# Optimization experiments

Measured on AMD Instinct MI355X. Metric: run time of the kernel, lower is better.

The kernel has to match this reference:

```python
import jax, jax.numpy as jnp
import numpy as np

S = 100  # spatial_encoding_size

def setup_inputs() -> dict:
    key = jax.random.key(0)
    k1, k2 = jax.random.split(key)
    N, C, B = 1000000, 64, 32
    agent_encodings = jax.random.normal(k1, (N, C), dtype=jnp.float32)
    encode_coordinates = jax.random.randint(k2, (N,), 0, B * S * S, dtype=jnp.int64)
    return {"batch_size": B, "agent_encodings": agent_encodings, "encode_coordinates": encode_coordinates}

def reference(batch_size, agent_encodings, encode_coordinates):
    N, C = agent_encodings.shape
    num_seg = batch_size * S * S
    # max over all agents mapped to each flat grid cell (-inf for empty cells)
    seg_max = jax.ops.segment_max(agent_encodings, encode_coordinates, num_segments=num_seg)
    counts = jax.ops.segment_sum(jnp.ones((N,), dtype=agent_encodings.dtype), encode_coordinates, num_segments=num_seg)
    occupied = counts > 0
    grid = jnp.where(occupied[:, None], seg_max, jnp.zeros((), dtype=agent_encodings.dtype))
    grid = grid.reshape(batch_size, S, S, C)
    return jnp.transpose(grid, (0, 3, 1, 2))  # [B, C, S, S]
```

## Files before the change

### kernel.cpp

```cpp
#include <hip/hip_runtime.h>
#include <math.h>


#define S_DIM 100
#define CELLS_PER_B (S_DIM * S_DIM)
#define C_DIM 64

__global__ void build_lists(const int* __restrict__ coords,
                            int* __restrict__ head, int* __restrict__ next,
                            int n) {
    const int stride = gridDim.x * blockDim.x;
    for (int i = blockIdx.x * blockDim.x + threadIdx.x; i < n; i += stride) {
        const int c = coords[i];
        next[i] = atomicExch(&head[c], i);
    }
}

__global__ void gather_max(const float* __restrict__ enc,
                           const int* __restrict__ head,
                           const int* __restrict__ next,
                           float* __restrict__ out, int ncells) {
    __shared__ float tile[16][C_DIM + 1];
    const int tid = threadIdx.x;
    const int cl = tid >> 4;
    const int c4 = (tid & 15) << 2;
    const int cell = blockIdx.x * 16 + cl;

    float4 m = make_float4(-INFINITY, -INFINITY, -INFINITY, -INFINITY);
    int agent = (cell < ncells) ? head[cell] : -1;
    const bool occupied = (agent >= 0);
    while (agent >= 0) {
        const float4 v =
            *reinterpret_cast<const float4*>(enc + (size_t)agent * C_DIM + c4);
        m.x = fmaxf(m.x, v.x);
        m.y = fmaxf(m.y, v.y);
        m.z = fmaxf(m.z, v.z);
        m.w = fmaxf(m.w, v.w);
        agent = next[agent];
    }
    if (!occupied) m = make_float4(0.f, 0.f, 0.f, 0.f);
    tile[cl][c4 + 0] = m.x;
    tile[cl][c4 + 1] = m.y;
    tile[cl][c4 + 2] = m.z;
    tile[cl][c4 + 3] = m.w;
    __syncthreads();

    const int cell0 = blockIdx.x * 16;
    const int b = cell0 / CELLS_PER_B;
    const int rem0 = cell0 - b * CELLS_PER_B;
    float* base = out + ((size_t)b * C_DIM) * CELLS_PER_B + rem0;
    for (int i = tid; i < 16 * C_DIM; i += 256) {
        const int c = i >> 4;
        const int j = i & 15;
        if (cell0 + j < ncells)
            base[(size_t)c * CELLS_PER_B + j] = tile[j][c];
    }
}

__device__ __forceinline__ unsigned encode_f32(float f) {
    unsigned u = __float_as_uint(f);
    return (u & 0x80000000u) ? ~u : (u | 0x80000000u);
}
__device__ __forceinline__ float decode_key(unsigned k) {
    if (k == 0u) return 0.0f;
    return (k & 0x80000000u) ? __uint_as_float(k & 0x7FFFFFFFu)
                             : __uint_as_float(~k);
}
__global__ void spatial_scatter_max(const float* __restrict__ enc,
                                    const int* __restrict__ coords,
                                    unsigned* __restrict__ grid,
                                    int n_agents, int C) {
    const long long total = (long long)n_agents * 16;
    const long long stride = (long long)gridDim.x * blockDim.x;
    for (long long i = (long long)blockIdx.x * blockDim.x + threadIdx.x;
         i < total; i += stride) {
        const int agent = (int)(i >> 4);
        const int c4 = ((int)i & 15) << 2;
        const int coord = coords[agent];
        const int b = coord / CELLS_PER_B;
        const int rem = coord - b * CELLS_PER_B;
        const float4 v =
            *reinterpret_cast<const float4*>(enc + (size_t)agent * C + c4);
        unsigned* p = grid + ((size_t)b * C + c4) * CELLS_PER_B + rem;
        atomicMax(p, encode_f32(v.x));
        atomicMax(p + 1 * CELLS_PER_B, encode_f32(v.y));
        atomicMax(p + 2 * CELLS_PER_B, encode_f32(v.z));
        atomicMax(p + 3 * CELLS_PER_B, encode_f32(v.w));
    }
}
__global__ void spatial_decode(unsigned* __restrict__ grid, int n4) {
    const int stride = gridDim.x * blockDim.x;
    uint4* g4 = reinterpret_cast<uint4*>(grid);
    for (int i = blockIdx.x * blockDim.x + threadIdx.x; i < n4; i += stride) {
        uint4 k = g4[i];
        float4 f;
        f.x = decode_key(k.x);
        f.y = decode_key(k.y);
        f.z = decode_key(k.z);
        f.w = decode_key(k.w);
        reinterpret_cast<float4*>(g4)[i] = f;
    }
}

extern "C" void kernel_launch(void* const* d_in, const int* in_sizes, int n_in,
                              void* d_out, int out_size, void* d_ws, size_t ws_size,
                              hipStream_t stream) {
    const float* enc = (const float*)d_in[1];
    const int* coords = (const int*)d_in[2];
    const int n = in_sizes[2];
    const int ncells = out_size / C_DIM;

    const size_t need = (size_t)ncells * 4 + (size_t)n * 4;
    if (ws_size >= need) {
        int* head = (int*)d_ws;
        int* next = head + ncells;
        hipMemsetAsync(head, 0xFF, (size_t)ncells * 4, stream);
        build_lists<<<2048, 256, 0, stream>>>(coords, head, next, n);
        gather_max<<<(ncells + 15) / 16, 256, 0, stream>>>(
            enc, head, next, (float*)d_out, ncells);
    } else {
        unsigned* out = (unsigned*)d_out;
        hipMemsetAsync(d_out, 0, (size_t)out_size * sizeof(float), stream);
        spatial_scatter_max<<<2048, 256, 0, stream>>>(enc, coords, out, n,
                                                      C_DIM);
        spatial_decode<<<2048, 256, 0, stream>>>(out, out_size / 4);
    }
}
```

Measured before the change: 131.5 us.

## Widen gather tiles to 32 cells, use 2D grid, prefetch next pointer

The gather kernel now handles 32 cells per 512-thread block on a 2D grid indexed by batch and cell chunk, so each channel row is written in 32-float contiguous runs and no integer division is needed. It also loads the next-pointer before the encoding row, so walking the linked list overlaps with the feature load. The memset is replaced by a small init kernel and the atomic-scatter fallback is removed, which assumes the workspace is always large enough. Tiles that span the boundary between batches are now clipped correctly.

After: 132.5 us. About the same (+0.7%).

```diff
diff --git a/kernel.cpp b/kernel.cpp
--- a/kernel.cpp
+++ b/kernel.cpp
@@ -5,6 +5,13 @@
 #define S_DIM 100
 #define CELLS_PER_B (S_DIM * S_DIM)
 #define C_DIM 64
+#define CPB 32
+
+__global__ void init_head(int* __restrict__ head, int n) {
+    const int stride = gridDim.x * blockDim.x;
+    for (int i = blockIdx.x * blockDim.x + threadIdx.x; i < n; i += stride)
+        head[i] = -1;
+}
 
 __global__ void build_lists(const int* __restrict__ coords,
                             int* __restrict__ head, int* __restrict__ next,
@@ -16,27 +23,29 @@
     }
 }
 
-__global__ void gather_max(const float* __restrict__ enc,
-                           const int* __restrict__ head,
-                           const int* __restrict__ next,
-                           float* __restrict__ out, int ncells) {
-    __shared__ float tile[16][C_DIM + 1];
+__global__ __launch_bounds__(512) void gather_max(
+    const float* __restrict__ enc, const int* __restrict__ head,
+    const int* __restrict__ next, float* __restrict__ out) {
+    __shared__ float tile[CPB][C_DIM + 1];
     const int tid = threadIdx.x;
     const int cl = tid >> 4;
     const int c4 = (tid & 15) << 2;
-    const int cell = blockIdx.x * 16 + cl;
+    const int b = blockIdx.y;
+    const int rem0 = blockIdx.x * CPB;
+    const int rem = rem0 + cl;
 
     float4 m = make_float4(-INFINITY, -INFINITY, -INFINITY, -INFINITY);
-    int agent = (cell < ncells) ? head[cell] : -1;
+    int agent = (rem < CELLS_PER_B) ? head[b * CELLS_PER_B + rem] : -1;
     const bool occupied = (agent >= 0);
     while (agent >= 0) {
+        const int nxt = next[agent];
         const float4 v =
             *reinterpret_cast<const float4*>(enc + (size_t)agent * C_DIM + c4);
         m.x = fmaxf(m.x, v.x);
         m.y = fmaxf(m.y, v.y);
         m.z = fmaxf(m.z, v.z);
         m.w = fmaxf(m.w, v.w);
-        agent = next[agent];
+        agent = nxt;
     }
     if (!occupied) m = make_float4(0.f, 0.f, 0.f, 0.f);
     tile[cl][c4 + 0] = m.x;
@@ -45,60 +54,12 @@
     tile[cl][c4 + 3] = m.w;
     __syncthreads();
 
-    const int cell0 = blockIdx.x * 16;
-    const int b = cell0 / CELLS_PER_B;
-    const int rem0 = cell0 - b * CELLS_PER_B;
     float* base = out + ((size_t)b * C_DIM) * CELLS_PER_B + rem0;
-    for (int i = tid; i < 16 * C_DIM; i += 256) {
-        const int c = i >> 4;
-        const int j = i & 15;
-        if (cell0 + j < ncells)
-            base[(size_t)c * CELLS_PER_B + j] = tile[j][c];
-    }
-}
-
-__device__ __forceinline__ unsigned encode_f32(float f) {
-    unsigned u = __float_as_uint(f);
-    return (u & 0x80000000u) ? ~u : (u | 0x80000000u);
-}
-__device__ __forceinline__ float decode_key(unsigned k) {
-    if (k == 0u) return 0.0f;
-    return (k & 0x80000000u) ? __uint_as_float(k & 0x7FFFFFFFu)
-                             : __uint_as_float(~k);
-}
-__global__ void spatial_scatter_max(const float* __restrict__ enc,
-                                    const int* __restrict__ coords,
-                                    unsigned* __restrict__ grid,
-                                    int n_agents, int C) {
-    const long long total = (long long)n_agents * 16;
-    const long long stride = (long long)gridDim.x * blockDim.x;
-    for (long long i = (long long)blockIdx.x * blockDim.x + threadIdx.x;
-         i < total; i += stride) {
-        const int agent = (int)(i >> 4);
-        const int c4 = ((int)i & 15) << 2;
-        const int coord = coords[agent];
-        const int b = coord / CELLS_PER_B;
-        const int rem = coord - b * CELLS_PER_B;
-        const float4 v =
-            *reinterpret_cast<const float4*>(enc + (size_t)agent * C + c4);
-        unsigned* p = grid + ((size_t)b * C + c4) * CELLS_PER_B + rem;
-        atomicMax(p, encode_f32(v.x));
-        atomicMax(p + 1 * CELLS_PER_B, encode_f32(v.y));
-        atomicMax(p + 2 * CELLS_PER_B, encode_f32(v.z));
-        atomicMax(p + 3 * CELLS_PER_B, encode_f32(v.w));
-    }
-}
-__global__ void spatial_decode(unsigned* __restrict__ grid, int n4) {
-    const int stride = gridDim.x * blockDim.x;
-    uint4* g4 = reinterpret_cast<uint4*>(grid);
-    for (int i = blockIdx.x * blockDim.x + threadIdx.x; i < n4; i += stride) {
-        uint4 k = g4[i];
-        float4 f;
-        f.x = decode_key(k.x);
-        f.y = decode_key(k.y);
-        f.z = decode_key(k.z);
-        f.w = decode_key(k.w);
-        reinterpret_cast<float4*>(g4)[i] = f;
+    const int limit = min(CPB, CELLS_PER_B - rem0);
+    for (int i = tid; i < CPB * C_DIM; i += 512) {
+        const int c = i >> 5;
+        const int j = i & 31;
+        if (j < limit) base[(size_t)c * CELLS_PER_B + j] = tile[j][c];
     }
 }
 
@@ -109,20 +70,13 @@
     const int* coords = (const int*)d_in[2];
     const int n = in_sizes[2];
     const int ncells = out_size / C_DIM;
+    const int B = ncells / CELLS_PER_B;
 
-    const size_t need = (size_t)ncells * 4 + (size_t)n * 4;
-    if (ws_size >= need) {
-        int* head = (int*)d_ws;
-        int* next = head + ncells;
-        hipMemsetAsync(head, 0xFF, (size_t)ncells * 4, stream);
-        build_lists<<<2048, 256, 0, stream>>>(coords, head, next, n);
-        gather_max<<<(ncells + 15) / 16, 256, 0, stream>>>(
-            enc, head, next, (float*)d_out, ncells);
-    } else {
-        unsigned* out = (unsigned*)d_out;
-        hipMemsetAsync(d_out, 0, (size_t)out_size * sizeof(float), stream);
-        spatial_scatter_max<<<2048, 256, 0, stream>>>(enc, coords, out, n,
-                                                      C_DIM);
-        spatial_decode<<<2048, 256, 0, stream>>>(out, out_size / 4);
-    }
+    int* head = (int*)d_ws;
+    int* next = head + ncells;
+
+    init_head<<<1024, 256, 0, stream>>>(head, ncells);
+    build_lists<<<2048, 256, 0, stream>>>(coords, head, next, n);
+    dim3 grid((CELLS_PER_B + CPB - 1) / CPB, B);
+    gather_max<<<grid, 512, 0, stream>>>(enc, head, next, (float*)d_out);
 }
```
